# Kernel optimization log

Measured on AMD Instinct MI355X. Metric: run time of the kernel, lower is better.

Reference implementation:

```python
import jax, jax.numpy as jnp
import numpy as np

B, N, DIM, H = 8, 1024, 1024, 8
HEAD_DIM = DIM // H
SCALE = HEAD_DIM ** -0.5  # scale_with_head=True


def setup_inputs() -> dict:
    key = jax.random.key(0)
    k1, k2, k3, k4 = jax.random.split(key, 4)
    return {
        "q": jax.random.normal(k1, (B, N, DIM), dtype=jnp.float32),
        "k": jax.random.normal(k2, (B, N, DIM), dtype=jnp.float32),
        "v": jax.random.normal(k3, (B, N, DIM), dtype=jnp.float32),
        "W_out": jax.random.normal(k4, (DIM, DIM), dtype=jnp.float32) * (DIM ** -0.5),
        "b_out": jnp.zeros((DIM,), dtype=jnp.float32),
    }


def reference(q, k, v, W_out, b_out):
    b, n, dim = q.shape
    h, d = H, dim // H
    # b n (h d) -> b h n d
    def split_heads(t):
        return t.reshape(b, n, h, d).transpose(0, 2, 1, 3)
    qh, kh, vh = split_heads(q), split_heads(k), split_heads(v)
    dots = jnp.einsum('bhid,bhjd->bhij', qh, kh) * SCALE
    attn = jax.nn.softmax(dots, axis=-1)
    out = jnp.einsum('bhij,bhjd->bhid', attn, vh)
    out = out.transpose(0, 2, 1, 3).reshape(b, n, dim)  # b h n d -> b n (h d)
    out = out @ W_out.T + b_out  # nn.Linear(dim, dim); dropout p=0 is identity
    return out, attn
```

## Files before the change

### kernel.cpp

```cpp
#include <hip/hip_runtime.h>

typedef __bf16 bf16x8 __attribute__((ext_vector_type(8)));
typedef unsigned short u16x8 __attribute__((ext_vector_type(8)));
typedef unsigned short u16x4 __attribute__((ext_vector_type(4)));
typedef float f32x4 __attribute__((ext_vector_type(4)));
typedef float f32x16 __attribute__((ext_vector_type(16)));

#define B_    8
#define N_    1024
#define DIM_  1024
#define H_    8
#define HD_   128
#define SCALE_ 0.08838834764831845f

__device__ __forceinline__ unsigned short f2bf(float x) {
  unsigned int u = __float_as_uint(x);
  u += 0x7fffu + ((u >> 16) & 1u);
  return (unsigned short)(u >> 16);
}
__device__ __forceinline__ float bf2f(unsigned short h) {
  return __uint_as_float(((unsigned int)h) << 16);
}
__device__ __forceinline__ f32x4 mfma16(u16x8 a, u16x8 b, f32x4 c) {
  return __builtin_amdgcn_mfma_f32_16x16x32_bf16(
      __builtin_bit_cast(bf16x8, a), __builtin_bit_cast(bf16x8, b), c, 0, 0, 0);
}
__device__ __forceinline__ f32x16 mfma32(u16x8 a, u16x8 b, f32x16 c) {
  return __builtin_amdgcn_mfma_f32_32x32x16_bf16(
      __builtin_bit_cast(bf16x8, a), __builtin_bit_cast(bf16x8, b), c, 0, 0, 0);
}
__device__ __forceinline__ void gl_lds16(const void* g, void* l) {
  __builtin_amdgcn_global_load_lds(
      (const __attribute__((address_space(1))) unsigned int*)g,
      (__attribute__((address_space(3))) unsigned int*)l, 16, 0, 0);
}
#define SBAR() do { asm volatile("" ::: "memory"); __builtin_amdgcn_s_barrier(); \
                    asm volatile("" ::: "memory"); } while (0)
#define LGKM0() do { asm volatile("s_waitcnt lgkmcnt(0)" ::: "memory"); \
                     __builtin_amdgcn_sched_barrier(0); } while (0)
#define VMC(n)  asm volatile("s_waitcnt vmcnt(" #n ")" ::: "memory")

#define WS_KIMG  ((size_t)0)
#define WS_VIMG  ((size_t)32 << 20)
#define WS_WIMG  ((size_t)64 << 20)
#define WS_AOIMG ((size_t)68 << 20)

__global__ __launch_bounds__(256)
void prep_all(const float* __restrict__ gk, const float* __restrict__ gv,
              const float* __restrict__ gw, char* __restrict__ kimg,
              char* __restrict__ vimg, char* __restrict__ wimg) {
  const int blk = blockIdx.x;
  const int t = threadIdx.x;
  if (blk < 1024) {
    const int bh = blk >> 4, it = blk & 15;
    const int bb = bh >> 3, hh = bh & 7;
    char* base = kimg + (size_t)bh * 524288 + it * 32768;
    const float* src = gk + ((size_t)bb * N_ + it * 64) * DIM_ + hh * HD_;
    #pragma unroll
    for (int c = 0; c < 8; ++c) {
      const int idx = t + 256 * c;
      const int key = idx >> 5, dq = (idx & 31) * 4;
      f32x4 f = *(const f32x4*)(src + (size_t)key * DIM_ + dq);
      u16x4 h, g;
      #pragma unroll
      for (int j = 0; j < 4; ++j) {
        unsigned short hv = f2bf(f[j]);
        h[j] = hv;
        g[j] = f2bf(f[j] - bf2f(hv));
      }
      const int dh = dq >> 6, dloc = dq & 63;
      const int off = (dloc * 2) ^ ((key & 7) << 4);
      char* dst = base + dh * 16384 + key * 256;
      *(u16x4*)(dst + off) = h;
      *(u16x4*)(dst + 128 + off) = g;
    }
  } else if (blk < 3072) {
    __shared__ float tile[32][132];
    const int b2 = blk - 1024;
    const int bh = b2 >> 5, kt = b2 & 31;
    const int bb = bh >> 3, hh = bh & 7;
    const float* src = gv + ((size_t)bb * N_ + kt * 32) * DIM_ + hh * HD_;
    #pragma unroll
    for (int c = 0; c < 4; ++c) {
      const int idx = t + 256 * c;
      const int key = idx >> 5, dq = (idx & 31) * 4;
      *(f32x4*)&tile[key][dq] = *(const f32x4*)(src + (size_t)key * DIM_ + dq);
    }
    __syncthreads();
    char* base = vimg + (size_t)bh * 524288 + kt * 16384;
    #pragma unroll
    for (int c = 0; c < 2; ++c) {
      const int oc = t + 256 * c;
      const int d = oc >> 2, kc = oc & 3;
      u16x8 h, g;
      #pragma unroll
      for (int j = 0; j < 8; ++j) {
        float x = tile[kc * 8 + j][d];
        unsigned short hv = f2bf(x);
        h[j] = hv;
        g[j] = f2bf(x - bf2f(hv));
      }
      const int off = (d * 64 + kc * 16) ^ ((d & 7) << 4);
      *(u16x8*)(base + off) = h;
      *(u16x8*)(base + 8192 + off) = g;
    }
  } else {
    const int idx = (blk - 3072) * 256 + t;
    const int n = idx >> 7, k0 = (idx & 127) * 8;
    const float* s = gw + (size_t)n * DIM_ + k0;
    f32x4 f0 = *(const f32x4*)s;
    f32x4 f1 = *(const f32x4*)(s + 4);
    u16x8 h, g;
    #pragma unroll
    for (int j = 0; j < 8; ++j) {
      float x = j < 4 ? f0[j] : f1[j - 4];
      unsigned short hv = f2bf(x);
      h[j] = hv;
      g[j] = f2bf(x - bf2f(hv));
    }
    const int T = (n >> 7) * 32 + (k0 >> 5);
    const int rl = n & 127, kl = k0 & 31;
    char* base = wimg + (size_t)T * 16384 + rl * 128;
    const int swz = (rl & 7) << 4;
    *(u16x8*)(base + ((kl * 2) ^ swz)) = h;
    *(u16x8*)(base + ((64 + kl * 2) ^ swz)) = g;
  }
}

struct K1Smem {
  unsigned short p[64 * 1024];
  union {
    char kb[2][16384];
    char vt[2][16384];
    char comb[8][4096];
    struct { char pad[16384]; float partial[4][64]; float rinv[64]; } pp;
  } u;
};

__global__ __launch_bounds__(1024, 4)
void attn_kernel(const float* __restrict__ gq, const char* __restrict__ kimg,
                 const char* __restrict__ vimg, float* __restrict__ gattn,
                 char* __restrict__ aoimg) {
  __shared__ K1Smem sm;
  const int bid = blockIdx.x;
  const int xcd = bid & 7, slot = bid >> 3;
  const int bh = xcd + 8 * (slot >> 4);
  const int qt = slot & 15;
  const int bb = bh >> 3, hh = bh & 7;

  const int tid = threadIdx.x;
  const int wid = tid >> 6, lane = tid & 63;
  const int rg = wid >> 2;
  const int kg = wid & 3;
  const int l15 = lane & 15, l4 = lane >> 4;
  const int prg = wid >> 3;
  const int pkg = wid & 3;
  const int pkh = (wid >> 2) & 1;
  const int l31 = lane & 31, l5 = lane >> 5;

  const char* kimg_bh = kimg + (size_t)bh * 524288;
  const char* vimg_bh = vimg + (size_t)bh * 524288;

  auto issueK = [&](int s) {
    const char* src = kimg_bh + s * 16384 + wid * 1024 + lane * 16;
    gl_lds16(src, sm.u.kb[s & 1] + wid * 1024);
  };
  auto issueV = [&](int kt) {
    const char* src = vimg_bh + kt * 16384 + wid * 1024 + lane * 16;
    gl_lds16(src, sm.u.vt[kt & 1] + wid * 1024);
  };

  issueK(0);

  u16x8 qhi[4], qlo[4];
  {
    const int qrow = qt * 64 + rg * 16 + l15;
    const float* qp = gq + ((size_t)bb * N_ + qrow) * DIM_ + hh * HD_;
    #pragma unroll
    for (int t = 0; t < 4; ++t) {
      const int d0 = t * 32 + l4 * 8;
      f32x4 f0 = *(const f32x4*)(qp + d0);
      f32x4 f1 = *(const f32x4*)(qp + d0 + 4);
      #pragma unroll
      for (int j = 0; j < 8; ++j) {
        float x = (j < 4 ? f0[j] : f1[j - 4]) * SCALE_;
        unsigned short hi = f2bf(x);
        qhi[t][j] = hi;
        qlo[t][j] = f2bf(x - bf2f(hi));
      }
    }
  }

  issueK(1);
  VMC(1);
  SBAR();

  float lsum = 0.f;
  const int key16 = kg * 16 + l15;
  const int kswz = (key16 & 7) << 4;
  const char* krow0 = sm.u.kb[0] + key16 * 256;
  const char* krow1 = sm.u.kb[1] + key16 * 256;
  const int prow_i = rg * 16 + l15;
  char* const prow = (char*)sm.p + prow_i * 2048;
  const int pswz = (prow_i & 7) << 4;

  f32x4 a0, a1, a2;
  #pragma unroll 2
  for (int s = 0; s < 32; ++s) {
    const int dh = s & 1;
    if (s >= 1 && s < 31) issueK(s + 1);
    else if (s == 31) issueV(0);
    const char* krow = dh ? krow1 : krow0;
    u16x8 khi[2], klo[2];
    #pragma unroll
    for (int tl = 0; tl < 2; ++tl) {
      const int off = (tl * 64 + l4 * 16) ^ kswz;
      khi[tl] = *(const u16x8*)(krow + off);
      klo[tl] = *(const u16x8*)(krow + 128 + off);
    }
    if (dh == 0) {
      a0 = f32x4{0.f, 0.f, 0.f, 0.f};
      a1 = f32x4{0.f, 0.f, 0.f, 0.f};
      a2 = f32x4{0.f, 0.f, 0.f, 0.f};
    }
    __builtin_amdgcn_s_setprio(1);
    #pragma unroll
    for (int tl = 0; tl < 2; ++tl) {
      const int t = dh * 2 + tl;
      a0 = mfma16(khi[tl], qhi[t], a0);
      a1 = mfma16(klo[tl], qhi[t], a1);
      a2 = mfma16(khi[tl], qlo[t], a2);
    }
    __builtin_amdgcn_s_setprio(0);
    if (dh == 1) {
      const int keyb = ((s >> 1) * 64 + kg * 16 + l4 * 4) * 2;
      u16x4 pk;
      float ls = 0.f;
      #pragma unroll
      for (int r = 0; r < 4; ++r) {
        float sv = (a0[r] + a1[r]) + a2[r];
        sv = fminf(sv, 60.0f);
        float p = __expf(sv);
        ls += p;
        pk[r] = f2bf(p);
      }
      lsum += ls;
      *(u16x4*)(prow + (keyb ^ pswz)) = pk;
    }
    if (s < 31) { VMC(0); }
    else       { VMC(2); }
    SBAR();
  }

  {
    float s0 = lsum;
    s0 += __shfl_xor(s0, 16);
    s0 += __shfl_xor(s0, 32);
    if (lane < 16) sm.u.pp.partial[kg][rg * 16 + lane] = s0;
  }
  LGKM0();
  SBAR();
  if (tid < 64) {
    float t4 = sm.u.pp.partial[0][tid] + sm.u.pp.partial[1][tid] +
               sm.u.pp.partial[2][tid] + sm.u.pp.partial[3][tid];
    sm.u.pp.rinv[tid] = 1.0f / t4;
  }
  LGKM0();
  SBAR();
  const bool wr8 = (wid < 8);
  const int wrow = wid * 8 + (lane >> 3);
  const float rvs = sm.u.pp.rinv[wrow & 63];
  float rv16[16];
  if (pkh == 0) {
    #pragma unroll
    for (int r = 0; r < 16; ++r) {
      const int rowreg = (r & 3) + 8 * (r >> 2) + 4 * l5;
      rv16[r] = sm.u.pp.rinv[prg * 32 + rowreg];
    }
  }
  LGKM0();
  VMC(0);
  SBAR();

  f32x16 acc = {};
  const char* pArow = (const char*)sm.p + (prg * 32 + l31) * 2048;
  const int paswz = ((prg * 32 + l31) & 7) << 4;
  const char* wprow = (const char*)sm.p + wrow * 2048;
  const int wswz = (wrow & 7) << 4;
  float* wdst = gattn + ((size_t)bh * N_ + qt * 64 + wrow) * N_ + (lane & 7) * 4;
  const int dpv = pkg * 32 + l31;
  const int voff = (dpv * 64 + pkh * 32 + l5 * 16) ^ ((dpv & 7) << 4);

  #pragma unroll 2
  for (int kt = 0; kt < 32; ++kt) {
    if (kt < 31) issueV(kt + 1);
    const char* vbase = sm.u.vt[kt & 1];
    u16x8 vh = *(const u16x8*)(vbase + voff);
    u16x8 vl = *(const u16x8*)(vbase + 8192 + voff);
    u16x8 pa = *(const u16x8*)(pArow + ((kt * 64 + pkh * 32 + l5 * 16) ^ paswz));
    __builtin_amdgcn_s_setprio(1);
    acc = mfma32(pa, vh, acc);
    acc = mfma32(pa, vl, acc);
    __builtin_amdgcn_s_setprio(0);
    if (wr8) {
      u16x4 pw = *(const u16x4*)(wprow + ((kt * 64 + (lane & 7) * 8) ^ wswz));
      f32x4 o;
      o[0] = bf2f(pw[0]) * rvs; o[1] = bf2f(pw[1]) * rvs;
      o[2] = bf2f(pw[2]) * rvs; o[3] = bf2f(pw[3]) * rvs;
      __builtin_nontemporal_store(o, (f32x4*)(wdst + kt * 32));
    }
    LGKM0();
    if (kt < 31) {
      if (wr8) { VMC(1); }
      else     { VMC(0); }
    }
    SBAR();
  }

  {
    char* cbase = sm.u.comb[prg * 4 + pkg] + lane * 64;
    if (pkh == 1) {
      #pragma unroll
      for (int q = 0; q < 4; ++q) {
        f32x4 v = {acc[q * 4], acc[q * 4 + 1], acc[q * 4 + 2], acc[q * 4 + 3]};
        *(f32x4*)(cbase + q * 16) = v;
      }
    }
    LGKM0();
    SBAR();
    if (pkh == 0) {
      #pragma unroll
      for (int q = 0; q < 4; ++q) {
        f32x4 v = *(const f32x4*)(cbase + q * 16);
        acc[q * 4] += v[0]; acc[q * 4 + 1] += v[1];
        acc[q * 4 + 2] += v[2]; acc[q * 4 + 3] += v[3];
      }
      const int col5 = hh * 4 + pkg;
      const int mt = bb * 8 + (qt >> 1);
      char* Tbase = aoimg + ((size_t)(mt * 32 + col5)) * 16384;
      const int klb = l31 * 2;
      #pragma unroll
      for (int r = 0; r < 16; ++r) {
        const int rowreg = (r & 3) + 8 * (r >> 2) + 4 * l5;
        const int rl = (qt & 1) * 64 + prg * 32 + rowreg;
        const int swz = (rl & 7) << 4;
        float val = acc[r] * rv16[r];
        unsigned short hv = f2bf(val);
        unsigned short lv = f2bf(val - bf2f(hv));
        char* rp = Tbase + rl * 128;
        __builtin_nontemporal_store(hv, (unsigned short*)(rp + (klb ^ swz)));
        __builtin_nontemporal_store(lv, (unsigned short*)(rp + ((64 + klb) ^ swz)));
      }
    }
  }
}

struct K2Smem {
  char A[2][16384];
  char Bm[2][16384];
};

__global__ __launch_bounds__(512, 2)
void proj_kernel(const char* __restrict__ aoimg, const char* __restrict__ wimg,
                 const float* __restrict__ gbias, float* __restrict__ gout) {
  __shared__ K2Smem sm;
  const int nt = blockIdx.x & 7;
  const int mt = blockIdx.x >> 3;
  const int tid = threadIdx.x;
  const int wid = tid >> 6, lane = tid & 63;
  const int wr = wid >> 2, wc = wid & 3;
  const int l15 = lane & 15, l4 = lane >> 4;

  auto issue = [&](int s) {
    const char* sa = aoimg + ((size_t)(mt * 32 + s)) * 16384 + tid * 16;
    gl_lds16(sa, sm.A[s & 1] + (tid >> 6) * 1024);
    gl_lds16(sa + 8192, sm.A[s & 1] + 8192 + (tid >> 6) * 1024);
    const char* sb = wimg + ((size_t)(nt * 32 + s)) * 16384 + tid * 16;
    gl_lds16(sb, sm.Bm[s & 1] + (tid >> 6) * 1024);
    gl_lds16(sb + 8192, sm.Bm[s & 1] + 8192 + (tid >> 6) * 1024);
  };

  f32x4 acc[4][2];
  #pragma unroll
  for (int i = 0; i < 4; ++i)
    #pragma unroll
    for (int j = 0; j < 2; ++j) acc[i][j] = f32x4{0.f, 0.f, 0.f, 0.f};

  issue(0);
  VMC(0);
  SBAR();
  #pragma unroll 1
  for (int s = 0; s < 32; ++s) {
    if (s < 31) issue(s + 1);
    const char* Ab = sm.A[s & 1];
    const char* Bb = sm.Bm[s & 1];
    u16x8 ah[4], al[4], bh[2], bl[2];
    #pragma unroll
    for (int rt = 0; rt < 4; ++rt) {
      const int rl = wr * 64 + rt * 16 + l15;
      const char* rp = Ab + rl * 128;
      const int swz = (rl & 7) << 4;
      ah[rt] = *(const u16x8*)(rp + ((l4 * 16) ^ swz));
      al[rt] = *(const u16x8*)(rp + ((64 + l4 * 16) ^ swz));
    }
    #pragma unroll
    for (int ct = 0; ct < 2; ++ct) {
      const int cl = wc * 32 + ct * 16 + l15;
      const char* rp = Bb + cl * 128;
      const int swz = (cl & 7) << 4;
      bh[ct] = *(const u16x8*)(rp + ((l4 * 16) ^ swz));
      bl[ct] = *(const u16x8*)(rp + ((64 + l4 * 16) ^ swz));
    }
    __builtin_amdgcn_s_setprio(1);
    #pragma unroll
    for (int rt = 0; rt < 4; ++rt)
      #pragma unroll
      for (int ct = 0; ct < 2; ++ct)
        acc[rt][ct] = mfma16(ah[rt], bh[ct], acc[rt][ct]);
    #pragma unroll
    for (int rt = 0; rt < 4; ++rt)
      #pragma unroll
      for (int ct = 0; ct < 2; ++ct)
        acc[rt][ct] = mfma16(ah[rt], bl[ct], acc[rt][ct]);
    #pragma unroll
    for (int rt = 0; rt < 4; ++rt)
      #pragma unroll
      for (int ct = 0; ct < 2; ++ct)
        acc[rt][ct] = mfma16(al[rt], bh[ct], acc[rt][ct]);
    __builtin_amdgcn_s_setprio(0);
    LGKM0();
    if (s < 31) VMC(0);
    SBAR();
  }

  #pragma unroll
  for (int ct = 0; ct < 2; ++ct) {
    const int col = nt * 128 + wc * 32 + ct * 16 + l15;
    const float bv = gbias[col];
    #pragma unroll
    for (int rt = 0; rt < 4; ++rt) {
      float* dst = gout + (size_t)(mt * 128 + wr * 64 + rt * 16 + l4 * 4) * DIM_ + col;
      #pragma unroll
      for (int r = 0; r < 4; ++r)
        dst[(size_t)r * DIM_] = acc[rt][ct][r] + bv;
    }
  }
}

extern "C" void kernel_launch(void* const* d_in, const int* in_sizes, int n_in,
                              void* d_out, int out_size, void* d_ws, size_t ws_size,
                              hipStream_t stream) {
  const float* q    = (const float*)d_in[0];
  const float* k    = (const float*)d_in[1];
  const float* v    = (const float*)d_in[2];
  const float* W    = (const float*)d_in[3];
  const float* bias = (const float*)d_in[4];
  float* out  = (float*)d_out;
  float* attn = out + (size_t)B_ * N_ * DIM_;

  char* ws = (char*)d_ws;
  char* kimg  = ws + WS_KIMG;
  char* vimg  = ws + WS_VIMG;
  char* wimg  = ws + WS_WIMG;
  char* aoimg = ws + WS_AOIMG;

  prep_all<<<3584, 256, 0, stream>>>(k, v, W, kimg, vimg, wimg);
  attn_kernel<<<B_ * H_ * (N_ / 64), 1024, 0, stream>>>(q, kimg, vimg, attn, aoimg);
  proj_kernel<<<512, 512, 0, stream>>>(aoimg, wimg, bias, out);
}
```

Before: 243.4 us.

## Split K/V hi-lo images; stage only hi parts in LDS, load lo from global

The prep kernel now writes the bf16 high and low halves of K and V into separate workspace images. The low halves are laid out in MFMA-fragment order so each lane can load them straight into registers from global/L2. Only the high halves are streamed into LDS, which halves the LDS traffic and the K/V staging buffers. The QK loop now covers a whole 64-key tile per iteration with one barrier, and only the upper 8 waves issue the V loads. The cost is extra per-lane global loads that sit on the MFMA critical path, plus changed wait and barrier logic that could expose latency.

New measurement: 275.3 us. 1.13x slower.

```diff
diff --git a/kernel.cpp b/kernel.cpp
--- a/kernel.cpp
+++ b/kernel.cpp
@@ -40,27 +40,31 @@
                      __builtin_amdgcn_sched_barrier(0); } while (0)
 #define VMC(n)  asm volatile("s_waitcnt vmcnt(" #n ")" ::: "memory")
 
-#define WS_KIMG  ((size_t)0)
-#define WS_VIMG  ((size_t)32 << 20)
+#define WS_KHI   ((size_t)0)
+#define WS_KLO   ((size_t)16 << 20)
+#define WS_VH    ((size_t)32 << 20)
+#define WS_VL    ((size_t)48 << 20)
 #define WS_WIMG  ((size_t)64 << 20)
 #define WS_AOIMG ((size_t)68 << 20)
 
 __global__ __launch_bounds__(256)
 void prep_all(const float* __restrict__ gk, const float* __restrict__ gv,
-              const float* __restrict__ gw, char* __restrict__ kimg,
-              char* __restrict__ vimg, char* __restrict__ wimg) {
+              const float* __restrict__ gw, char* __restrict__ khi_g,
+              char* __restrict__ klo_g, char* __restrict__ vh_g,
+              char* __restrict__ vl_g, char* __restrict__ wimg) {
   const int blk = blockIdx.x;
   const int t = threadIdx.x;
   if (blk < 1024) {
-    const int bh = blk >> 4, it = blk & 15;
+    const int bh = blk >> 4, tile = blk & 15;
     const int bb = bh >> 3, hh = bh & 7;
-    char* base = kimg + (size_t)bh * 524288 + it * 32768;
-    const float* src = gk + ((size_t)bb * N_ + it * 64) * DIM_ + hh * HD_;
+    char* hbase = khi_g + (size_t)bh * 262144 + tile * 16384;
+    char* lbase = klo_g + (size_t)bh * 262144;
+    const float* src = gk + ((size_t)bb * N_ + tile * 64) * DIM_ + hh * HD_;
     #pragma unroll
     for (int c = 0; c < 8; ++c) {
       const int idx = t + 256 * c;
-      const int key = idx >> 5, dq = (idx & 31) * 4;
-      f32x4 f = *(const f32x4*)(src + (size_t)key * DIM_ + dq);
+      const int key = idx >> 5, d0 = (idx & 31) * 4;
+      f32x4 f = *(const f32x4*)(src + (size_t)key * DIM_ + d0);
       u16x4 h, g;
       #pragma unroll
       for (int j = 0; j < 4; ++j) {
@@ -68,11 +72,12 @@
         h[j] = hv;
         g[j] = f2bf(f[j] - bf2f(hv));
       }
-      const int dh = dq >> 6, dloc = dq & 63;
-      const int off = (dloc * 2) ^ ((key & 7) << 4);
-      char* dst = base + dh * 16384 + key * 256;
-      *(u16x4*)(dst + off) = h;
-      *(u16x4*)(dst + 128 + off) = g;
+      *(u16x4*)(hbase + key * 256 + ((d0 * 2) ^ ((key & 7) << 4))) = h;
+      const int kg = key >> 4, l15 = key & 15;
+      const int d8 = d0 >> 3, t2 = d8 >> 2, l4q = d8 & 3;
+      const int sub8 = (d0 & 4) * 2;
+      char* bp = lbase + (((tile * 4 + kg) * 4 + t2) << 10) + (l4q * 16 + l15) * 16 + sub8;
+      *(u16x4*)bp = g;
     }
   } else if (blk < 3072) {
     __shared__ float tile[32][132];
@@ -87,22 +92,24 @@
       *(f32x4*)&tile[key][dq] = *(const f32x4*)(src + (size_t)key * DIM_ + dq);
     }
     __syncthreads();
-    char* base = vimg + (size_t)bh * 524288 + kt * 16384;
+    char* hbase = vh_g + (size_t)bh * 262144 + kt * 8192;
+    char* lbase = vl_g + (size_t)bh * 262144;
     #pragma unroll
     for (int c = 0; c < 2; ++c) {
       const int oc = t + 256 * c;
-      const int d = oc >> 2, kc = oc & 3;
+      const int d = oc >> 2, k8 = oc & 3;
       u16x8 h, g;
       #pragma unroll
       for (int j = 0; j < 8; ++j) {
-        float x = tile[kc * 8 + j][d];
+        float x = tile[k8 * 8 + j][d];
         unsigned short hv = f2bf(x);
         h[j] = hv;
         g[j] = f2bf(x - bf2f(hv));
       }
-      const int off = (d * 64 + kc * 16) ^ ((d & 7) << 4);
-      *(u16x8*)(base + off) = h;
-      *(u16x8*)(base + 8192 + off) = g;
+      *(u16x8*)(hbase + ((d * 64 + k8 * 16) ^ ((d & 7) << 4))) = h;
+      const int pkg = d >> 5, l31 = d & 31, pkh = k8 >> 1, l5 = k8 & 1;
+      char* bp = lbase + (((kt * 4 + pkg) * 2 + pkh) << 10) + (l5 * 32 + l31) * 16;
+      *(u16x8*)bp = g;
     }
   } else {
     const int idx = (blk - 3072) * 256 + t;
@@ -131,15 +138,16 @@
   unsigned short p[64 * 1024];
   union {
     char kb[2][16384];
-    char vt[2][16384];
+    char vt[2][8192];
     char comb[8][4096];
     struct { char pad[16384]; float partial[4][64]; float rinv[64]; } pp;
   } u;
 };
 
 __global__ __launch_bounds__(1024, 4)
-void attn_kernel(const float* __restrict__ gq, const char* __restrict__ kimg,
-                 const char* __restrict__ vimg, float* __restrict__ gattn,
+void attn_kernel(const float* __restrict__ gq, const char* __restrict__ khi_g,
+                 const char* __restrict__ klo_g, const char* __restrict__ vh_g,
+                 const char* __restrict__ vl_g, float* __restrict__ gattn,
                  char* __restrict__ aoimg) {
   __shared__ K1Smem sm;
   const int bid = blockIdx.x;
@@ -158,16 +166,18 @@
   const int pkh = (wid >> 2) & 1;
   const int l31 = lane & 31, l5 = lane >> 5;
 
-  const char* kimg_bh = kimg + (size_t)bh * 524288;
-  const char* vimg_bh = vimg + (size_t)bh * 524288;
+  const char* khi_bh = khi_g + (size_t)bh * 262144;
+  const char* klo_bh = klo_g + (size_t)bh * 262144;
+  const char* vh_bh  = vh_g + (size_t)bh * 262144;
+  const char* vl_bh  = vl_g + (size_t)bh * 262144;
 
   auto issueK = [&](int s) {
-    const char* src = kimg_bh + s * 16384 + wid * 1024 + lane * 16;
+    const char* src = khi_bh + s * 16384 + wid * 1024 + lane * 16;
     gl_lds16(src, sm.u.kb[s & 1] + wid * 1024);
   };
   auto issueV = [&](int kt) {
-    const char* src = vimg_bh + kt * 16384 + wid * 1024 + lane * 16;
-    gl_lds16(src, sm.u.vt[kt & 1] + wid * 1024);
+    const char* src = vh_bh + kt * 8192 + (wid - 8) * 1024 + lane * 16;
+    gl_lds16(src, sm.u.vt[kt & 1] + (wid - 8) * 1024);
   };
 
   issueK(0);
@@ -198,42 +208,37 @@
   float lsum = 0.f;
   const int key16 = kg * 16 + l15;
   const int kswz = (key16 & 7) << 4;
-  const char* krow0 = sm.u.kb[0] + key16 * 256;
-  const char* krow1 = sm.u.kb[1] + key16 * 256;
   const int prow_i = rg * 16 + l15;
   char* const prow = (char*)sm.p + prow_i * 2048;
   const int pswz = (prow_i & 7) << 4;
 
-  f32x4 a0, a1, a2;
-  #pragma unroll 2
-  for (int s = 0; s < 32; ++s) {
-    const int dh = s & 1;
-    if (s >= 1 && s < 31) issueK(s + 1);
-    else if (s == 31) issueV(0);
-    const char* krow = dh ? krow1 : krow0;
-    u16x8 khi[2], klo[2];
-    #pragma unroll
-    for (int tl = 0; tl < 2; ++tl) {
-      const int off = (tl * 64 + l4 * 16) ^ kswz;
-      khi[tl] = *(const u16x8*)(krow + off);
-      klo[tl] = *(const u16x8*)(krow + 128 + off);
-    }
-    if (dh == 0) {
-      a0 = f32x4{0.f, 0.f, 0.f, 0.f};
-      a1 = f32x4{0.f, 0.f, 0.f, 0.f};
-      a2 = f32x4{0.f, 0.f, 0.f, 0.f};
-    }
+  #pragma unroll 1
+  for (int s = 0; s < 16; ++s) {
+    if (s < 15) issueK(s + 1);
+    const char* kloblk = klo_bh + (((s * 4 + kg) * 4) << 10) + lane * 16;
+    u16x8 klo0 = *(const u16x8*)(kloblk);
+    u16x8 klo1 = *(const u16x8*)(kloblk + 1024);
+    u16x8 klo2 = *(const u16x8*)(kloblk + 2048);
+    u16x8 klo3 = *(const u16x8*)(kloblk + 3072);
+    const char* krow = sm.u.kb[s & 1] + key16 * 256;
+    u16x8 khi[4];
+    #pragma unroll
+    for (int t = 0; t < 4; ++t)
+      khi[t] = *(const u16x8*)(krow + ((t * 64 + l4 * 16) ^ kswz));
+    f32x4 a0 = {0.f, 0.f, 0.f, 0.f}, a1 = a0, a2 = a0;
     __builtin_amdgcn_s_setprio(1);
     #pragma unroll
-    for (int tl = 0; tl < 2; ++tl) {
-      const int t = dh * 2 + tl;
-      a0 = mfma16(khi[tl], qhi[t], a0);
-      a1 = mfma16(klo[tl], qhi[t], a1);
-      a2 = mfma16(khi[tl], qlo[t], a2);
-    }
+    for (int t = 0; t < 4; ++t) {
+      a0 = mfma16(khi[t], qhi[t], a0);
+      a2 = mfma16(khi[t], qlo[t], a2);
+    }
+    a1 = mfma16(klo0, qhi[0], a1);
+    a1 = mfma16(klo1, qhi[1], a1);
+    a1 = mfma16(klo2, qhi[2], a1);
+    a1 = mfma16(klo3, qhi[3], a1);
     __builtin_amdgcn_s_setprio(0);
-    if (dh == 1) {
-      const int keyb = ((s >> 1) * 64 + kg * 16 + l4 * 4) * 2;
+    {
+      const int keyb = (s * 64 + kg * 16 + l4 * 4) * 2;
       u16x4 pk;
       float ls = 0.f;
       #pragma unroll
@@ -247,11 +252,11 @@
       lsum += ls;
       *(u16x4*)(prow + (keyb ^ pswz)) = pk;
     }
-    if (s < 31) { VMC(0); }
-    else       { VMC(2); }
+    if (s < 15) VMC(0);
     SBAR();
   }
 
+  if (wid >= 8) issueV(0);
   {
     float s0 = lsum;
     s0 += __shfl_xor(s0, 16);
@@ -268,8 +273,8 @@
   LGKM0();
   SBAR();
   const bool wr8 = (wid < 8);
-  const int wrow = wid * 8 + (lane >> 3);
-  const float rvs = sm.u.pp.rinv[wrow & 63];
+  const int wrow = (wid & 7) * 8 + (lane >> 3);
+  const float rvs = sm.u.pp.rinv[wrow];
   float rv16[16];
   if (pkh == 0) {
     #pragma unroll
@@ -279,7 +284,7 @@
     }
   }
   LGKM0();
-  VMC(0);
+  if (wid >= 8) VMC(0);
   SBAR();
 
   f32x16 acc = {};
@@ -290,13 +295,13 @@
   float* wdst = gattn + ((size_t)bh * N_ + qt * 64 + wrow) * N_ + (lane & 7) * 4;
   const int dpv = pkg * 32 + l31;
   const int voff = (dpv * 64 + pkh * 32 + l5 * 16) ^ ((dpv & 7) << 4);
+  const char* vlbase = vl_bh + (((pkg * 2 + pkh)) << 10) + (l5 * 32 + l31) * 16;
 
   #pragma unroll 2
   for (int kt = 0; kt < 32; ++kt) {
-    if (kt < 31) issueV(kt + 1);
-    const char* vbase = sm.u.vt[kt & 1];
-    u16x8 vh = *(const u16x8*)(vbase + voff);
-    u16x8 vl = *(const u16x8*)(vbase + 8192 + voff);
+    if (wid >= 8 && kt < 31) issueV(kt + 1);
+    u16x8 vl = *(const u16x8*)(vlbase + (kt << 13));
+    u16x8 vh = *(const u16x8*)(sm.u.vt[kt & 1] + voff);
     u16x8 pa = *(const u16x8*)(pArow + ((kt * 64 + pkh * 32 + l5 * 16) ^ paswz));
     __builtin_amdgcn_s_setprio(1);
     acc = mfma32(pa, vh, acc);
@@ -308,11 +313,8 @@
       o[0] = bf2f(pw[0]) * rvs; o[1] = bf2f(pw[1]) * rvs;
       o[2] = bf2f(pw[2]) * rvs; o[3] = bf2f(pw[3]) * rvs;
       __builtin_nontemporal_store(o, (f32x4*)(wdst + kt * 32));
-    }
-    LGKM0();
-    if (kt < 31) {
-      if (wr8) { VMC(1); }
-      else     { VMC(0); }
+    } else if (kt < 31) {
+      VMC(0);
     }
     SBAR();
   }
@@ -459,12 +461,14 @@
   float* attn = out + (size_t)B_ * N_ * DIM_;
 
   char* ws = (char*)d_ws;
-  char* kimg  = ws + WS_KIMG;
-  char* vimg  = ws + WS_VIMG;
+  char* khi_g = ws + WS_KHI;
+  char* klo_g = ws + WS_KLO;
+  char* vh_g  = ws + WS_VH;
+  char* vl_g  = ws + WS_VL;
   char* wimg  = ws + WS_WIMG;
   char* aoimg = ws + WS_AOIMG;
 
-  prep_all<<<3584, 256, 0, stream>>>(k, v, W, kimg, vimg, wimg);
-  attn_kernel<<<B_ * H_ * (N_ / 64), 1024, 0, stream>>>(q, kimg, vimg, attn, aoimg);
+  prep_all<<<3584, 256, 0, stream>>>(k, v, W, khi_g, klo_g, vh_g, vl_g, wimg);
+  attn_kernel<<<B_ * H_ * (N_ / 64), 1024, 0, stream>>>(q, khi_g, klo_g, vh_g, vl_g, attn, aoimg);
   proj_kernel<<<512, 512, 0, stream>>>(aoimg, wimg, bias, out);
 }
```

## Restructure QK^T phase: each wave handles 32 query rows over 128-key chunks

Applied to the files above, without the earlier changes.

The K image layout changes from 64-key tiles split by head-dim half to 128-key chunks split into four 32-dim quarters, so each staged tile covers 128 keys. In the QK^T loop each wave now owns 32 query rows (two 16-row blocks) and 16 keys across 8 key groups. Each K fragment loaded from shared memory is reused for both query blocks, roughly halving LDS reads per MFMA. The cost is twice the Q registers and accumulators, a wider 8-way partial-sum reduction, and a barrier per quarter step, which could raise register pressure at 1024 threads.

Measured after the change: 292.1 us. 1.2x slower.

```diff
diff --git a/kernel.cpp b/kernel.cpp
--- a/kernel.cpp
+++ b/kernel.cpp
@@ -54,13 +54,13 @@
   if (blk < 1024) {
     const int bh = blk >> 4, it = blk & 15;
     const int bb = bh >> 3, hh = bh & 7;
-    char* base = kimg + (size_t)bh * 524288 + it * 32768;
+    char* base = kimg + (size_t)bh * 524288;
     const float* src = gk + ((size_t)bb * N_ + it * 64) * DIM_ + hh * HD_;
     #pragma unroll
     for (int c = 0; c < 8; ++c) {
       const int idx = t + 256 * c;
-      const int key = idx >> 5, dq = (idx & 31) * 4;
-      f32x4 f = *(const f32x4*)(src + (size_t)key * DIM_ + dq);
+      const int key_in = idx >> 5, dq = (idx & 31) * 4;
+      f32x4 f = *(const f32x4*)(src + (size_t)key_in * DIM_ + dq);
       u16x4 h, g;
       #pragma unroll
       for (int j = 0; j < 4; ++j) {
@@ -68,11 +68,13 @@
         h[j] = hv;
         g[j] = f2bf(f[j] - bf2f(hv));
       }
-      const int dh = dq >> 6, dloc = dq & 63;
-      const int off = (dloc * 2) ^ ((key & 7) << 4);
-      char* dst = base + dh * 16384 + key * 256;
-      *(u16x4*)(dst + off) = h;
-      *(u16x4*)(dst + 128 + off) = g;
+      const int kk = it * 64 + key_in;
+      const int cch = kk >> 7, key_loc = kk & 127;
+      const int qq = dq >> 5, dloc = dq & 31;
+      char* dst = base + (cch * 4 + qq) * 16384 + key_loc * 128;
+      const int swz = (key_loc & 7) << 4;
+      *(u16x4*)(dst + ((dloc * 2) ^ swz)) = h;
+      *(u16x4*)(dst + ((64 + dloc * 2) ^ swz)) = g;
     }
   } else if (blk < 3072) {
     __shared__ float tile[32][132];
@@ -133,7 +135,7 @@
     char kb[2][16384];
     char vt[2][16384];
     char comb[8][4096];
-    struct { char pad[16384]; float partial[4][64]; float rinv[64]; } pp;
+    struct { char pad[16384]; float partial[8][64]; float rinv[64]; } pp;
   } u;
 };
 
@@ -150,8 +152,8 @@
 
   const int tid = threadIdx.x;
   const int wid = tid >> 6, lane = tid & 63;
-  const int rg = wid >> 2;
-  const int kg = wid & 3;
+  const int rg = wid >> 3;
+  const int kg = wid & 7;
   const int l15 = lane & 15, l4 = lane >> 4;
   const int prg = wid >> 3;
   const int pkg = wid & 3;
@@ -172,9 +174,10 @@
 
   issueK(0);
 
-  u16x8 qhi[4], qlo[4];
-  {
-    const int qrow = qt * 64 + rg * 16 + l15;
+  u16x8 qhi[2][4], qlo[2][4];
+  #pragma unroll
+  for (int bi = 0; bi < 2; ++bi) {
+    const int qrow = qt * 64 + rg * 32 + bi * 16 + l15;
     const float* qp = gq + ((size_t)bb * N_ + qrow) * DIM_ + hh * HD_;
     #pragma unroll
     for (int t = 0; t < 4; ++t) {
@@ -185,8 +188,8 @@
       for (int j = 0; j < 8; ++j) {
         float x = (j < 4 ? f0[j] : f1[j - 4]) * SCALE_;
         unsigned short hi = f2bf(x);
-        qhi[t][j] = hi;
-        qlo[t][j] = f2bf(x - bf2f(hi));
+        qhi[bi][t][j] = hi;
+        qlo[bi][t][j] = f2bf(x - bf2f(hi));
       }
     }
   }
@@ -195,81 +198,89 @@
   VMC(1);
   SBAR();
 
-  float lsum = 0.f;
-  const int key16 = kg * 16 + l15;
-  const int kswz = (key16 & 7) << 4;
-  const char* krow0 = sm.u.kb[0] + key16 * 256;
-  const char* krow1 = sm.u.kb[1] + key16 * 256;
-  const int prow_i = rg * 16 + l15;
-  char* const prow = (char*)sm.p + prow_i * 2048;
-  const int pswz = (prow_i & 7) << 4;
-
-  f32x4 a0, a1, a2;
-  #pragma unroll 2
+  float lsum0 = 0.f, lsum1 = 0.f;
+  const int key_loc = kg * 16 + l15;
+  const int kswz = (key_loc & 7) << 4;
+  const int krowoff = key_loc * 128;
+  const int prow0_i = rg * 32 + l15;
+  const int prow1_i = rg * 32 + 16 + l15;
+  char* const prow0 = (char*)sm.p + prow0_i * 2048;
+  char* const prow1 = (char*)sm.p + prow1_i * 2048;
+  const int pswz = (prow0_i & 7) << 4;
+
+  f32x4 a0[2], a1[2], a2[2];
+  #pragma unroll 4
   for (int s = 0; s < 32; ++s) {
-    const int dh = s & 1;
-    if (s >= 1 && s < 31) issueK(s + 1);
-    else if (s == 31) issueV(0);
-    const char* krow = dh ? krow1 : krow0;
-    u16x8 khi[2], klo[2];
-    #pragma unroll
-    for (int tl = 0; tl < 2; ++tl) {
-      const int off = (tl * 64 + l4 * 16) ^ kswz;
-      khi[tl] = *(const u16x8*)(krow + off);
-      klo[tl] = *(const u16x8*)(krow + 128 + off);
-    }
-    if (dh == 0) {
-      a0 = f32x4{0.f, 0.f, 0.f, 0.f};
-      a1 = f32x4{0.f, 0.f, 0.f, 0.f};
-      a2 = f32x4{0.f, 0.f, 0.f, 0.f};
+    const int q = s & 3;
+    if (s < 31) issueK(s + 1);
+    else issueV(0);
+    const char* krow = sm.u.kb[s & 1] + krowoff;
+    u16x8 khi = *(const u16x8*)(krow + ((l4 * 16) ^ kswz));
+    u16x8 klo = *(const u16x8*)(krow + ((64 + l4 * 16) ^ kswz));
+    if (q == 0) {
+      #pragma unroll
+      for (int bi = 0; bi < 2; ++bi) {
+        a0[bi] = f32x4{0.f, 0.f, 0.f, 0.f};
+        a1[bi] = f32x4{0.f, 0.f, 0.f, 0.f};
+        a2[bi] = f32x4{0.f, 0.f, 0.f, 0.f};
+      }
     }
     __builtin_amdgcn_s_setprio(1);
     #pragma unroll
-    for (int tl = 0; tl < 2; ++tl) {
-      const int t = dh * 2 + tl;
-      a0 = mfma16(khi[tl], qhi[t], a0);
-      a1 = mfma16(klo[tl], qhi[t], a1);
-      a2 = mfma16(khi[tl], qlo[t], a2);
+    for (int bi = 0; bi < 2; ++bi) {
+      a0[bi] = mfma16(khi, qhi[bi][q], a0[bi]);
+      a1[bi] = mfma16(klo, qhi[bi][q], a1[bi]);
+      a2[bi] = mfma16(khi, qlo[bi][q], a2[bi]);
     }
     __builtin_amdgcn_s_setprio(0);
-    if (dh == 1) {
-      const int keyb = ((s >> 1) * 64 + kg * 16 + l4 * 4) * 2;
-      u16x4 pk;
-      float ls = 0.f;
-      #pragma unroll
-      for (int r = 0; r < 4; ++r) {
-        float sv = (a0[r] + a1[r]) + a2[r];
-        sv = fminf(sv, 60.0f);
-        float p = __expf(sv);
-        ls += p;
-        pk[r] = f2bf(p);
-      }
-      lsum += ls;
-      *(u16x4*)(prow + (keyb ^ pswz)) = pk;
-    }
-    if (s < 31) { VMC(0); }
-    else       { VMC(2); }
+    if (q == 3) {
+      const int keyb = ((s >> 2) * 128 + kg * 16 + l4 * 4) * 2;
+      #pragma unroll
+      for (int bi = 0; bi < 2; ++bi) {
+        u16x4 pk;
+        float ls = 0.f;
+        #pragma unroll
+        for (int r = 0; r < 4; ++r) {
+          float sv = (a0[bi][r] + a1[bi][r]) + a2[bi][r];
+          sv = fminf(sv, 60.0f);
+          float p = __expf(sv);
+          ls += p;
+          pk[r] = f2bf(p);
+        }
+        if (bi == 0) { lsum0 += ls; *(u16x4*)(prow0 + (keyb ^ pswz)) = pk; }
+        else         { lsum1 += ls; *(u16x4*)(prow1 + (keyb ^ pswz)) = pk; }
+      }
+    }
+    if (s < 31) VMC(0);
     SBAR();
   }
 
   {
-    float s0 = lsum;
+    float s0 = lsum0;
     s0 += __shfl_xor(s0, 16);
     s0 += __shfl_xor(s0, 32);
-    if (lane < 16) sm.u.pp.partial[kg][rg * 16 + lane] = s0;
+    float s1 = lsum1;
+    s1 += __shfl_xor(s1, 16);
+    s1 += __shfl_xor(s1, 32);
+    if (lane < 16) {
+      sm.u.pp.partial[kg][rg * 32 + lane] = s0;
+      sm.u.pp.partial[kg][rg * 32 + 16 + lane] = s1;
+    }
   }
   LGKM0();
   SBAR();
   if (tid < 64) {
     float t4 = sm.u.pp.partial[0][tid] + sm.u.pp.partial[1][tid] +
-               sm.u.pp.partial[2][tid] + sm.u.pp.partial[3][tid];
+               sm.u.pp.partial[2][tid] + sm.u.pp.partial[3][tid] +
+               sm.u.pp.partial[4][tid] + sm.u.pp.partial[5][tid] +
+               sm.u.pp.partial[6][tid] + sm.u.pp.partial[7][tid];
     sm.u.pp.rinv[tid] = 1.0f / t4;
   }
   LGKM0();
   SBAR();
   const bool wr8 = (wid < 8);
-  const int wrow = wid * 8 + (lane >> 3);
-  const float rvs = sm.u.pp.rinv[wrow & 63];
+  const int wrow = (wid & 7) * 8 + (lane >> 3);
+  const float rvs = sm.u.pp.rinv[wrow];
   float rv16[16];
   if (pkh == 0) {
     #pragma unroll
```

## Add dummy-load L2 prefetch of future K/V/W tiles and split V loads across waves

Applied to the files above, without the earlier changes.

Adds software prefetch loads, whose results are discarded into a sink register, that touch K/V image tiles several stages ahead in the attention kernel and A/W tiles three stages ahead in the projection kernel. The aim is to warm L2/MALL and hide global latency for the direct-to-LDS copies. V tile loads are also moved off the attention-probability writer waves and onto waves 8-15, each issuing two 1KB chunks, so the writers do not wait on V traffic. Wait counts are adjusted to account for the outstanding prefetch. The cost is extra load instructions, extra vmcnt bookkeeping, and some added memory traffic.

After: 277.6 us. +14.1%, slower.

```diff
diff --git a/kernel.cpp b/kernel.cpp
--- a/kernel.cpp
+++ b/kernel.cpp
@@ -52,10 +52,10 @@
   const int blk = blockIdx.x;
   const int t = threadIdx.x;
   if (blk < 1024) {
-    const int bh = blk >> 4, it = blk & 15;
+    const int bh = blk >> 4, tile = blk & 15;
     const int bb = bh >> 3, hh = bh & 7;
-    char* base = kimg + (size_t)bh * 524288 + it * 32768;
-    const float* src = gk + ((size_t)bb * N_ + it * 64) * DIM_ + hh * HD_;
+    char* base = kimg + (size_t)bh * 524288 + tile * 32768;
+    const float* src = gk + ((size_t)bb * N_ + tile * 64) * DIM_ + hh * HD_;
     #pragma unroll
     for (int c = 0; c < 8; ++c) {
       const int idx = t + 256 * c;
@@ -166,8 +166,10 @@
     gl_lds16(src, sm.u.kb[s & 1] + wid * 1024);
   };
   auto issueV = [&](int kt) {
-    const char* src = vimg_bh + kt * 16384 + wid * 1024 + lane * 16;
-    gl_lds16(src, sm.u.vt[kt & 1] + wid * 1024);
+    const char* src = vimg_bh + kt * 16384 + (wid - 8) * 2048 + lane * 16;
+    char* dst = sm.u.vt[kt & 1] + (wid - 8) * 2048;
+    gl_lds16(src, dst);
+    gl_lds16(src + 1024, dst + 1024);
   };
 
   issueK(0);
@@ -198,19 +200,21 @@
   float lsum = 0.f;
   const int key16 = kg * 16 + l15;
   const int kswz = (key16 & 7) << 4;
-  const char* krow0 = sm.u.kb[0] + key16 * 256;
-  const char* krow1 = sm.u.kb[1] + key16 * 256;
   const int prow_i = rg * 16 + l15;
   char* const prow = (char*)sm.p + prow_i * 2048;
   const int pswz = (prow_i & 7) << 4;
+  const bool kpf = (wid < 4);
+  const int pfidx = (wid * 64 + lane) * 64;
+  unsigned int pfv = 0, pfsink = 0;
 
   f32x4 a0, a1, a2;
   #pragma unroll 2
   for (int s = 0; s < 32; ++s) {
     const int dh = s & 1;
+    if (kpf) pfsink ^= pfv;
     if (s >= 1 && s < 31) issueK(s + 1);
-    else if (s == 31) issueV(0);
-    const char* krow = dh ? krow1 : krow0;
+    else if (s == 31) { if (wid >= 8) issueV(0); }
+    const char* krow = sm.u.kb[s & 1] + key16 * 256;
     u16x8 khi[2], klo[2];
     #pragma unroll
     for (int tl = 0; tl < 2; ++tl) {
@@ -247,10 +251,17 @@
       lsum += ls;
       *(u16x4*)(prow + (keyb ^ pswz)) = pk;
     }
-    if (s < 31) { VMC(0); }
-    else       { VMC(2); }
+    if (kpf) {
+      const char* pfa = (s < 28) ? (kimg_bh + (s + 4) * 16384 + pfidx)
+                                 : (vimg_bh + (s - 28) * 16384 + pfidx);
+      pfv = *(const unsigned int*)pfa;
+      if (s < 31) { VMC(1); } else { VMC(2); }
+    } else {
+      if (s < 31) { VMC(0); } else { VMC(2); }
+    }
     SBAR();
   }
+  if (kpf) pfsink ^= pfv;
 
   {
     float s0 = lsum;
@@ -268,8 +279,8 @@
   LGKM0();
   SBAR();
   const bool wr8 = (wid < 8);
-  const int wrow = wid * 8 + (lane >> 3);
-  const float rvs = sm.u.pp.rinv[wrow & 63];
+  const int wrow = (wid & 7) * 8 + (lane >> 3);
+  const float rvs = sm.u.pp.rinv[wrow];
   float rv16[16];
   if (pkh == 0) {
     #pragma unroll
@@ -290,10 +301,13 @@
   float* wdst = gattn + ((size_t)bh * N_ + qt * 64 + wrow) * N_ + (lane & 7) * 4;
   const int dpv = pkg * 32 + l31;
   const int voff = (dpv * 64 + pkh * 32 + l5 * 16) ^ ((dpv & 7) << 4);
+  const bool vpf = (wid >= 12);
+  const int vpfidx = ((wid - 12) * 64 + lane) * 64;
 
   #pragma unroll 2
   for (int kt = 0; kt < 32; ++kt) {
-    if (kt < 31) issueV(kt + 1);
+    if (vpf) pfsink ^= pfv;
+    if (wid >= 8 && kt < 31) issueV(kt + 1);
     const char* vbase = sm.u.vt[kt & 1];
     u16x8 vh = *(const u16x8*)(vbase + voff);
     u16x8 vl = *(const u16x8*)(vbase + 8192 + voff);
@@ -308,14 +322,17 @@
       o[0] = bf2f(pw[0]) * rvs; o[1] = bf2f(pw[1]) * rvs;
       o[2] = bf2f(pw[2]) * rvs; o[3] = bf2f(pw[3]) * rvs;
       __builtin_nontemporal_store(o, (f32x4*)(wdst + kt * 32));
+    } else if (vpf) {
+      if (kt < 27) pfv = *(const unsigned int*)(vimg_bh + (kt + 5) * 16384 + vpfidx);
+      if (kt < 31) { if (kt < 27) VMC(1); else VMC(0); }
+    } else {
+      if (kt < 31) VMC(0);
     }
     LGKM0();
-    if (kt < 31) {
-      if (wr8) { VMC(1); }
-      else     { VMC(0); }
-    }
     SBAR();
   }
+  if (vpf) pfsink ^= pfv;
+  asm volatile("" :: "v"(pfsink));
 
   {
     char* cbase = sm.u.comb[prg * 4 + pkg] + lane * 64;
@@ -379,6 +396,8 @@
     gl_lds16(sb, sm.Bm[s & 1] + (tid >> 6) * 1024);
     gl_lds16(sb + 8192, sm.Bm[s & 1] + 8192 + (tid >> 6) * 1024);
   };
+  const int pfidx = ((wid & 3) * 64 + lane) * 64;
+  unsigned int pfv = 0, pfsink = 0;
 
   f32x4 acc[4][2];
   #pragma unroll
@@ -391,6 +410,7 @@
   SBAR();
   #pragma unroll 1
   for (int s = 0; s < 32; ++s) {
+    pfsink ^= pfv;
     if (s < 31) issue(s + 1);
     const char* Ab = sm.A[s & 1];
     const char* Bb = sm.Bm[s & 1];
@@ -429,9 +449,19 @@
         acc[rt][ct] = mfma16(al[rt], bh[ct], acc[rt][ct]);
     __builtin_amdgcn_s_setprio(0);
     LGKM0();
-    if (s < 31) VMC(0);
+    if (s < 29) {
+      const char* pfa = (wid < 4)
+          ? (aoimg + ((size_t)(mt * 32 + s + 3)) * 16384 + pfidx)
+          : (wimg + ((size_t)(nt * 32 + s + 3)) * 16384 + pfidx);
+      pfv = *(const unsigned int*)pfa;
+      VMC(1);
+    } else if (s < 31) {
+      VMC(0);
+    }
     SBAR();
   }
+  pfsink ^= pfv;
+  asm volatile("" :: "v"(pfsink));
 
   #pragma unroll
   for (int ct = 0; ct < 2; ++ct) {
```
